# Kernel optimization log

Measured on AMD Instinct MI355X. Metric: run time of the kernel, lower is better.

## Reference

```python
import jax, jax.numpy as jnp
import numpy as np

NUM_CODES = 8192
CODE_DIM = 256
DECAY = 0.99
EPSILON = 1e-05
COMMITMENT_COST = 0.25


def setup_inputs() -> dict:
    key = jax.random.key(0)
    kz, ke = jax.random.split(key)
    z = jax.random.normal(kz, (8, 4096, CODE_DIM), dtype=jnp.float32)
    emb = jax.random.normal(ke, (NUM_CODES, CODE_DIM), dtype=jnp.float32)
    emb = emb / jnp.linalg.norm(emb, axis=1, keepdims=True)
    return {
        "z": z,
        "embedding": emb,
        "ema_cluster_size": jnp.zeros((NUM_CODES,), dtype=jnp.float32),
        "ema_embedding": emb,
    }


def reference(z, embedding, ema_cluster_size, ema_embedding):
    K, D = embedding.shape
    z_flat = z.reshape(-1, D)  # [N, D]
    # squared euclidean distances: [N, K]
    distances = (
        jnp.sum(z_flat * z_flat, axis=1, keepdims=True)
        - 2.0 * z_flat @ embedding.T
        + jnp.sum(embedding * embedding, axis=1)
    )
    indices = jnp.argmin(distances, axis=1)  # [N]
    z_q = embedding[indices]  # [N, D]

    # EMA update (training path); segment_sum replaces one-hot matmul scatter
    cluster_size = jax.ops.segment_sum(
        jnp.ones((z_flat.shape[0],), dtype=z_flat.dtype), indices, num_segments=K
    )
    new_ema_cluster_size = ema_cluster_size * DECAY + cluster_size * (1.0 - DECAY)
    dw = jax.ops.segment_sum(z_flat, indices, num_segments=K)  # [K, D]
    new_ema_embedding = ema_embedding * DECAY + dw * (1.0 - DECAY)
    n = jnp.sum(new_ema_cluster_size)
    smoothed = (new_ema_cluster_size + EPSILON) / (n + K * EPSILON) * n
    new_embedding = new_ema_embedding / smoothed[:, None]

    # straight-through (torch: z_q + (z_flat - z_q).detach())
    z_q_st = z_q + jax.lax.stop_gradient(z_flat - z_q)
    vq_loss = COMMITMENT_COST * jnp.mean((jax.lax.stop_gradient(z_q) - z_flat) ** 2)

    z_q_st = z_q_st.reshape(z.shape)
    indices = indices.reshape(z.shape[:-1])
    return (z_q_st, indices, vq_loss, new_embedding, new_ema_cluster_size, new_ema_embedding)
```

## Files before the change

### kernel.cpp

```cpp
#include <hip/hip_runtime.h>

#define NPTS   32768
#define NCODES 8192
#define DIM    256

#define DECAYF 0.99f
#define ONE_MINUS_DECAYF ((float)(1.0 - 0.99))
#define EPSF   1e-5f
#define KEPSF  ((float)(8192.0 * 1e-5))
#define MARGIN 0.05f

#define WS_PART  0
#define WS_A     (WS_PART + NPTS / 4 * 8)
#define WS_EN    (WS_A + NPTS * 4)
#define WS_CNT   (WS_EN + NCODES * 4)
#define WS_S     (WS_CNT + NCODES * 4)
#define WS_IDX   (WS_S + NCODES * 4)
#define WS_OFFS  (WS_IDX + NPTS * 4)
#define WS_CUR   (WS_OFFS + NCODES * 4)
#define WS_PLIST (WS_CUR + NCODES * 4)
#define WS_EMBT  (WS_PLIST + NPTS * 4)
#define WS_GMIN  (WS_EMBT + (size_t)DIM * NCODES * 4)
#define WS_AH    (WS_GMIN + (size_t)NPTS * 512 * 4)
#define WS_BH    (WS_AH + (size_t)NPTS * DIM * 2)

typedef __attribute__((ext_vector_type(8))) short short8;
typedef __attribute__((ext_vector_type(4))) float f32x4;

__device__ inline void gl_lds16(const void* g, void* l) {
    __builtin_amdgcn_global_load_lds(
        (const __attribute__((address_space(1))) void*)g,
        (__attribute__((address_space(3))) void*)l, 16, 0, 0);
}

__device__ inline unsigned short f2bf(float f) {
    unsigned u = __float_as_uint(f);
    return (unsigned short)((u + 0x7FFFu + ((u >> 16) & 1u)) >> 16);
}
__device__ inline unsigned f2ord(float f) {
    unsigned u = __float_as_uint(f);
    return (u & 0x80000000u) ? ~u : (u | 0x80000000u);
}

__global__ __launch_bounds__(256) void k_prep0(int* __restrict__ cnt) {
    int i = blockIdx.x * blockDim.x + threadIdx.x;
    if (i < NCODES) cnt[i] = 0;
}

__global__ __launch_bounds__(256) void k_rownorm(const float* __restrict__ x,
                                                 float* __restrict__ outn,
                                                 int nrows) {
    int w = (blockIdx.x * blockDim.x + threadIdx.x) >> 6;
    int lane = threadIdx.x & 63;
    if (w >= nrows) return;
    const float4 v = *(const float4*)(x + (size_t)w * DIM + 4 * lane);
    float q0 = v.x * v.x, q1 = v.y * v.y, q2 = v.z * v.z, q3 = v.w * v.w;
    double s = (double)q0 + (double)q1 + (double)q2 + (double)q3;
    #pragma unroll
    for (int off = 32; off > 0; off >>= 1) s += __shfl_down(s, off);
    if (lane == 0) outn[w] = (float)s;
}

__global__ __launch_bounds__(256) void k_split(const float* __restrict__ x,
                                               unsigned short* __restrict__ dst,
                                               int nelem) {
    int i = blockIdx.x * blockDim.x + threadIdx.x;
    int stride = gridDim.x * blockDim.x;
    for (int j = i; j < nelem; j += stride)
        dst[j] = f2bf(x[j]);
}

__global__ __launch_bounds__(512, 2) void k_gemm_argmin(
    const unsigned short* __restrict__ Ah,
    const unsigned short* __restrict__ Bh,
    const float* __restrict__ en,
    float* __restrict__ gmin);

template<int MH>
__device__ __forceinline__ void dsr_a(const unsigned short* LB, int wr, int l15,
                                      int l7, int quad, short8 (&af)[4][2]) {
#pragma unroll
    for (int m4 = 0; m4 < 4; ++m4) {
        const int r = wr * 128 + (MH * 4 + m4) * 16 + l15;
#pragma unroll
        for (int kk = 0; kk < 2; ++kk)
            af[m4][kk] = *(const short8*)&LB[(r * 8 + ((kk * 4 + quad) ^ l7)) * 8];
    }
}
template<int NH>
__device__ __forceinline__ void dsr_b(const unsigned short* LB, int wc, int l15,
                                      int l7, int quad, short8 (&bf)[2][2]) {
#pragma unroll
    for (int n2 = 0; n2 < 2; ++n2) {
        const int r = wc * 64 + (NH * 2 + n2) * 16 + l15;
#pragma unroll
        for (int kk = 0; kk < 2; ++kk)
            bf[n2][kk] = *(const short8*)&LB[16384 + (r * 8 + ((kk * 4 + quad) ^ l7)) * 8];
    }
}
template<int MH, int NH>
__device__ __forceinline__ void mma8(const short8 (&af)[4][2], const short8 (&bf)[2][2],
                                     f32x4 (&acc)[8][4]) {
#pragma unroll
    for (int m4 = 0; m4 < 4; ++m4)
#pragma unroll
        for (int n2 = 0; n2 < 2; ++n2)
#pragma unroll
            for (int kk = 0; kk < 2; ++kk)
                acc[MH * 4 + m4][NH * 2 + n2] = __builtin_amdgcn_mfma_f32_16x16x32_bf16(
                    af[m4][kk], bf[n2][kk], acc[MH * 4 + m4][NH * 2 + n2], 0, 0, 0);
}

__global__ __launch_bounds__(512, 2) void k_gemm_argmin(
    const unsigned short* __restrict__ Ah,
    const unsigned short* __restrict__ Bh,
    const float* __restrict__ en,
    float* __restrict__ gmin) {
    __shared__ __align__(16) unsigned short LDS[65536];

    const int t = threadIdx.x;
    const int w = t >> 6, l = t & 63;
    const int quad = l >> 4, l15 = l & 15, l7 = l & 7;
    const int wr = w >> 2, wc = w & 3;
    const int cb = blockIdx.x & 31, pb = blockIdx.x >> 5;
    const int cBase = cb * 256, pBase = pb * 256;

    const int lrs0 = t >> 3;
    const int xg = (t & 7) ^ (lrs0 & 7);
    const int rA0s0 = lrs0;
    const int rA0s1 = 128 + lrs0;
    const int rB0s0 = (lrs0 & 31) | ((lrs0 >> 5) << 6);
    const int rB0s1 = 128 + rB0s0;

    const unsigned short* gA0s0 = Bh + (size_t)(cBase + rA0s0) * DIM + xg * 8;
    const unsigned short* gA0s1 = Bh + (size_t)(cBase + rA0s1) * DIM + xg * 8;
    const unsigned short* gB0s0 = Ah + (size_t)(pBase + rB0s0) * DIM + xg * 8;
    const unsigned short* gB0s1 = Ah + (size_t)(pBase + rB0s1) * DIM + xg * 8;

    const int dA0s0 = (w * 8) * 64;
    const int dA0s1 = (128 + w * 8) * 64;
    const int dB0s0 = (((w & 3) * 8) | ((w >> 2) << 6)) * 64;
    const int dB0s1 = dB0s0 + 128 * 64;

#define STG_A0(KT, BUFS) do { \
        gl_lds16(gA0s0 + (KT) * 64, &LDS[(BUFS) + dA0s0]); \
        gl_lds16(gA0s1 + (KT) * 64, &LDS[(BUFS) + dA0s1]); } while (0)
#define STG_A1(KT, BUFS) do { \
        gl_lds16(gA0s0 + 64 * DIM + (KT) * 64, &LDS[(BUFS) + dA0s0 + 64 * 64]); \
        gl_lds16(gA0s1 + 64 * DIM + (KT) * 64, &LDS[(BUFS) + dA0s1 + 64 * 64]); } while (0)
#define STG_B0(KT, BUFS) do { \
        gl_lds16(gB0s0 + (KT) * 64, &LDS[(BUFS) + 16384 + dB0s0]); \
        gl_lds16(gB0s1 + (KT) * 64, &LDS[(BUFS) + 16384 + dB0s1]); } while (0)
#define STG_B1(KT, BUFS) do { \
        gl_lds16(gB0s0 + 32 * DIM + (KT) * 64, &LDS[(BUFS) + 16384 + dB0s0 + 32 * 64]); \
        gl_lds16(gB0s1 + 32 * DIM + (KT) * 64, &LDS[(BUFS) + 16384 + dB0s1 + 32 * 64]); } while (0)

    f32x4 acc[8][4];
#pragma unroll
    for (int i = 0; i < 8; ++i)
#pragma unroll
        for (int j = 0; j < 4; ++j) acc[i][j] = (f32x4){0.f, 0.f, 0.f, 0.f};

    STG_A0(0, 0); STG_B0(0, 0); STG_A1(0, 0); STG_B1(0, 0);
    STG_A0(1, 32768); STG_B0(1, 32768);
    asm volatile("s_waitcnt vmcnt(4)");
    __builtin_amdgcn_sched_barrier(0);
    __builtin_amdgcn_s_barrier();

    short8 af[4][2], bf0[2][2], bf1[2][2];
#pragma unroll
    for (int kt = 0; kt < 4; ++kt) {
        const unsigned short* LB = &LDS[(kt & 1) << 15];
        const int cbufS = (kt & 1) << 15;
        const int obufS = cbufS ^ 32768;
        dsr_a<0>(LB, wr, l15, l7, quad, af);
        dsr_b<0>(LB, wc, l15, l7, quad, bf0);
        if (kt + 1 < 4) STG_A1(kt + 1, obufS);
        __builtin_amdgcn_s_barrier();
        asm volatile("s_waitcnt lgkmcnt(0)");
        __builtin_amdgcn_sched_barrier(0);
        __builtin_amdgcn_s_setprio(1);
        mma8<0, 0>(af, bf0, acc);
        __builtin_amdgcn_s_setprio(0);
        __builtin_amdgcn_s_barrier();
        dsr_b<1>(LB, wc, l15, l7, quad, bf1);
        if (kt + 1 < 4) STG_B1(kt + 1, obufS);
        __builtin_amdgcn_s_barrier();
        asm volatile("s_waitcnt lgkmcnt(0)");
        __builtin_amdgcn_sched_barrier(0);
        __builtin_amdgcn_s_setprio(1);
        mma8<0, 1>(af, bf1, acc);
        __builtin_amdgcn_s_setprio(0);
        __builtin_amdgcn_s_barrier();
        dsr_a<1>(LB, wr, l15, l7, quad, af);
        if (kt + 2 < 4) STG_A0(kt + 2, cbufS);
        __builtin_amdgcn_s_barrier();
        asm volatile("s_waitcnt lgkmcnt(0)");
        __builtin_amdgcn_sched_barrier(0);
        __builtin_amdgcn_s_setprio(1);
        mma8<1, 0>(af, bf0, acc);
        __builtin_amdgcn_s_setprio(0);
        __builtin_amdgcn_s_barrier();
        if (kt + 2 < 4) STG_B0(kt + 2, cbufS);
        __builtin_amdgcn_s_barrier();
        __builtin_amdgcn_s_setprio(1);
        mma8<1, 1>(af, bf1, acc);
        __builtin_amdgcn_s_setprio(0);
        if (kt < 2) {
            asm volatile("s_waitcnt vmcnt(4)");
            __builtin_amdgcn_sched_barrier(0);
        } else if (kt == 2) {
            asm volatile("s_waitcnt vmcnt(0)");
            __builtin_amdgcn_sched_barrier(0);
        }
        __builtin_amdgcn_s_barrier();
    }
#undef STG_A0
#undef STG_A1
#undef STG_B0
#undef STG_B1

    float* outl = (float*)LDS;
#pragma unroll
    for (int m = 0; m < 8; ++m) {
        const float4 en4 = *(const float4*)&en[cBase + wr * 128 + m * 16 + quad * 4];
#pragma unroll
        for (int n = 0; n < 4; ++n) {
            f32x4 a = acc[m][n];
            float d0 = fmaf(-2.f, a[0], en4.x);
            float d1 = fmaf(-2.f, a[1], en4.y);
            float d2 = fmaf(-2.f, a[2], en4.z);
            float d3 = fmaf(-2.f, a[3], en4.w);
            float dm = fminf(fminf(d0, d1), fminf(d2, d3));
            dm = fminf(dm, __shfl_xor(dm, 16));
            dm = fminf(dm, __shfl_xor(dm, 32));
            if (quad == 0)
                outl[(wr * 8 + m) * 256 + wc * 64 + n * 16 + l15] = dm;
        }
    }
    __syncthreads();
    {
        const int pt = t >> 1, h = t & 1;
#pragma unroll
        for (int q2 = 0; q2 < 2; ++q2) {
            const int g0 = (h * 2 + q2) * 4;
            float4 v;
            v.x = outl[(g0 + 0) * 256 + pt];
            v.y = outl[(g0 + 1) * 256 + pt];
            v.z = outl[(g0 + 2) * 256 + pt];
            v.w = outl[(g0 + 3) * 256 + pt];
            *(float4*)&gmin[(size_t)(pBase + pt) * 512 + cb * 16 + g0] = v;
        }
    }
}

__global__ __launch_bounds__(256) void k_phase2(
    const float* __restrict__ z, const float* __restrict__ emb,
    const float* __restrict__ A, const float* __restrict__ en,
    const float* __restrict__ gmin,
    int* __restrict__ widx, float* __restrict__ out1,
    int* __restrict__ cnt) {
    int wpt = (blockIdx.x << 2) + (threadIdx.x >> 6);
    int l = threadIdx.x & 63;

    const float* gp = gmin + (size_t)wpt * 512;
    float loc[8];
    #pragma unroll
    for (int i = 0; i < 8; ++i) loc[i] = gp[i * 64 + l];
    float m8 = loc[0];
    #pragma unroll
    for (int i = 1; i < 8; ++i) m8 = fminf(m8, loc[i]);
    #pragma unroll
    for (int off = 1; off < 64; off <<= 1) m8 = fminf(m8, __shfl_xor(m8, off));
    const float thresh = m8 + MARGIN;

    const float4 z4 = *(const float4*)(z + (size_t)wpt * DIM + 4 * l);
    const float Azn = A[wpt];
    unsigned long long best = ~0ull;
    #pragma unroll 1
    for (int i = 0; i < 8; ++i) {
        unsigned long long mask = __ballot(loc[i] <= thresh);
        while (mask) {
            int s = __ffsll((long long)mask) - 1;
            mask &= mask - 1;
            int cbase = (i * 64 + s) << 4;
            #pragma unroll 4
            for (int k = 0; k < 16; ++k) {
                int c = cbase + k;
                const float4 ev = *(const float4*)(emb + (size_t)c * DIM + 4 * l);
                float p = fmaf(z4.x, ev.x,
                          fmaf(z4.y, ev.y,
                          fmaf(z4.z, ev.z, z4.w * ev.w)));
                #pragma unroll
                for (int off = 1; off < 64; off <<= 1) p += __shfl_xor(p, off);
                float dist = (Azn - 2.0f * p) + en[c];
                unsigned long long pk =
                    ((unsigned long long)f2ord(dist) << 32) | (unsigned)c;
                best = pk < best ? pk : best;
            }
        }
    }
    if (l == 0) {
        int idx = (int)(unsigned)best;
        widx[wpt] = idx;
        out1[wpt] = (float)idx;
        atomicAdd(cnt + idx, 1);
    }
}

__global__ __launch_bounds__(256) void k_scan(const int* __restrict__ cnt,
                                              const float* __restrict__ ecs,
                                              int* __restrict__ offs,
                                              int* __restrict__ cursor,
                                              float* __restrict__ out4,
                                              float* __restrict__ s_out) {
    __shared__ int ps[256];
    __shared__ double rd[256];
    __shared__ float nsh;
    int t = threadIdx.x;
    int base = t * 32;
    int loc[32];
    int s = 0;
    double nl = 0.0;
    #pragma unroll
    for (int i = 0; i < 32; ++i) {
        int c = cnt[base + i];
        loc[i] = c;
        s += c;
        float f = ecs[base + i] * DECAYF + (float)c * ONE_MINUS_DECAYF;
        out4[base + i] = f;
        nl += (double)f;
    }
    ps[t] = s;
    rd[t] = nl;
    __syncthreads();
    for (int off = 1; off < 256; off <<= 1) {
        int v = (t >= off) ? ps[t - off] : 0;
        __syncthreads();
        ps[t] += v;
        __syncthreads();
    }
    for (int off = 128; off > 0; off >>= 1) {
        if (t < off) rd[t] += rd[t + off];
        __syncthreads();
    }
    if (t == 0) nsh = (float)rd[0];
    __syncthreads();
    int run = (t == 0) ? 0 : ps[t - 1];
    #pragma unroll
    for (int i = 0; i < 32; ++i) {
        offs[base + i] = run;
        cursor[base + i] = run;
        run += loc[i];
    }
    float n = nsh;
    for (int k = t; k < NCODES; k += 256)
        s_out[k] = (out4[k] + EPSF) / (n + KEPSF) * n;
}

__global__ __launch_bounds__(256) void k_place(const int* __restrict__ widx,
                                               int* __restrict__ cursor,
                                               int* __restrict__ plist) {
    int p = blockIdx.x * 256 + threadIdx.x;
    int idx = widx[p];
    int slot = atomicAdd(&cursor[idx], 1);
    plist[slot] = p;
}

__global__ __launch_bounds__(256) void k_zq(const float* __restrict__ z,
                                            const float* __restrict__ emb,
                                            const int* __restrict__ widx,
                                            float* __restrict__ out0,
                                            double* __restrict__ part) {
    __shared__ double sred[4];
    int w = (blockIdx.x * blockDim.x + threadIdx.x) >> 6;
    int wv = threadIdx.x >> 6;
    int lane = threadIdx.x & 63;
    int idx = widx[w];
    const float4 zv = *(const float4*)(z + (size_t)w * DIM + 4 * lane);
    const float4 ev = *(const float4*)(emb + (size_t)idx * DIM + 4 * lane);

    float4 o;
    o.x = ev.x + (zv.x - ev.x);
    o.y = ev.y + (zv.y - ev.y);
    o.z = ev.z + (zv.z - ev.z);
    o.w = ev.w + (zv.w - ev.w);
    *(float4*)(out0 + (size_t)w * DIM + 4 * lane) = o;

    float t0 = ev.x - zv.x, t1 = ev.y - zv.y, t2 = ev.z - zv.z, t3 = ev.w - zv.w;
    float s0 = t0 * t0, s1 = t1 * t1, s2 = t2 * t2, s3 = t3 * t3;
    double ls = (double)s0 + (double)s1 + (double)s2 + (double)s3;
    #pragma unroll
    for (int off = 32; off > 0; off >>= 1) ls += __shfl_down(ls, off);
    if (lane == 0) sred[wv] = ls;
    __syncthreads();
    if (threadIdx.x == 0)
        part[blockIdx.x] = (sred[0] + sred[1]) + (sred[2] + sred[3]);
}

__global__ __launch_bounds__(256) void k_loss(const double* __restrict__ part,
                                              float* __restrict__ out2) {
    __shared__ double red[256];
    int t = threadIdx.x;
    double s = 0.0;
    for (int i = t; i < NPTS / 4; i += 256) s += part[i];
    red[t] = s;
    __syncthreads();
    for (int off = 128; off > 0; off >>= 1) {
        if (t < off) red[t] += red[t + off];
        __syncthreads();
    }
    if (t == 0)
        out2[0] = 0.25f * (float)(red[0] / (double)((size_t)NPTS * DIM));
}

__global__ __launch_bounds__(256) void k_dw(const float* __restrict__ z,
                                            const float* __restrict__ eem,
                                            const int* __restrict__ offs,
                                            const int* __restrict__ cnt,
                                            const int* __restrict__ plist,
                                            float* __restrict__ out5) {
    int c = blockIdx.x * 4 + (threadIdx.x >> 6);
    int lane = threadIdx.x & 63;
    int beg = offs[c], num = cnt[c];
    float4 acc = make_float4(0.f, 0.f, 0.f, 0.f);
    for (int j = 0; j < num; ++j) {
        int p = plist[beg + j];
        const float4 v = *(const float4*)(z + (size_t)p * DIM + 4 * lane);
        acc.x += v.x; acc.y += v.y; acc.z += v.z; acc.w += v.w;
    }
    const float4 e = *(const float4*)(eem + (size_t)c * DIM + 4 * lane);
    float4 o;
    o.x = e.x * DECAYF + acc.x * ONE_MINUS_DECAYF;
    o.y = e.y * DECAYF + acc.y * ONE_MINUS_DECAYF;
    o.z = e.z * DECAYF + acc.z * ONE_MINUS_DECAYF;
    o.w = e.w * DECAYF + acc.w * ONE_MINUS_DECAYF;
    *(float4*)(out5 + (size_t)c * DIM + 4 * lane) = o;
}

__global__ __launch_bounds__(256) void k_final(const float* __restrict__ out5,
                                               const float* __restrict__ s,
                                               float* __restrict__ out3) {
    int i = blockIdx.x * blockDim.x + threadIdx.x;
    int stride = gridDim.x * blockDim.x;
    for (int j = i; j < NCODES * DIM; j += stride)
        out3[j] = out5[j] / s[j >> 8];
}

extern "C" void kernel_launch(void* const* d_in, const int* in_sizes, int n_in,
                              void* d_out, int out_size, void* d_ws, size_t ws_size,
                              hipStream_t stream) {
    const float* z   = (const float*)d_in[0];
    const float* emb = (const float*)d_in[1];
    const float* ecs = (const float*)d_in[2];
    const float* eem = (const float*)d_in[3];

    float* out = (float*)d_out;
    float* out0 = out;
    float* out1 = out + 8388608;
    float* out2 = out + 8421376;
    float* out3 = out + 8421377;
    float* out4 = out + 10518529;
    float* out5 = out + 10526721;

    char* ws = (char*)d_ws;
    double* wPart = (double*)(ws + WS_PART);
    float*  wA    = (float*)(ws + WS_A);
    float*  wEn   = (float*)(ws + WS_EN);
    int*    wCnt  = (int*)(ws + WS_CNT);
    float*  wS    = (float*)(ws + WS_S);
    int*    wIdx  = (int*)(ws + WS_IDX);
    int*    wOffs = (int*)(ws + WS_OFFS);
    int*    wCur  = (int*)(ws + WS_CUR);
    int*    wPl   = (int*)(ws + WS_PLIST);
    float*  wGmin = (float*)(ws + WS_GMIN);
    unsigned short* wAh = (unsigned short*)(ws + WS_AH);
    unsigned short* wBh = (unsigned short*)(ws + WS_BH);

    hipLaunchKernelGGL(k_prep0, dim3(32), dim3(256), 0, stream, wCnt);
    hipLaunchKernelGGL(k_rownorm, dim3(NPTS / 4), dim3(256), 0, stream, z, wA, NPTS);
    hipLaunchKernelGGL(k_rownorm, dim3(NCODES / 4), dim3(256), 0, stream, emb, wEn, NCODES);
    hipLaunchKernelGGL(k_split, dim3(4096), dim3(256), 0, stream, z, wAh, NPTS * DIM);
    hipLaunchKernelGGL(k_split, dim3(1024), dim3(256), 0, stream, emb, wBh, NCODES * DIM);
    hipLaunchKernelGGL(k_gemm_argmin, dim3((NPTS / 256) * (NCODES / 256)), dim3(512), 0, stream,
                       wAh, wBh, wEn, wGmin);
    hipLaunchKernelGGL(k_phase2, dim3(NPTS / 4), dim3(256), 0, stream,
                       z, emb, wA, wEn, wGmin, wIdx, out1, wCnt);
    hipLaunchKernelGGL(k_scan, dim3(1), dim3(256), 0, stream,
                       wCnt, ecs, wOffs, wCur, out4, wS);
    hipLaunchKernelGGL(k_place, dim3(NPTS / 256), dim3(256), 0, stream, wIdx, wCur, wPl);
    hipLaunchKernelGGL(k_zq, dim3(NPTS / 4), dim3(256), 0, stream, z, emb, wIdx, out0, wPart);
    hipLaunchKernelGGL(k_loss, dim3(1), dim3(256), 0, stream, wPart, out2);
    hipLaunchKernelGGL(k_dw, dim3(NCODES / 4), dim3(256), 0, stream,
                       z, eem, wOffs, wCnt, wPl, out5);
    hipLaunchKernelGGL(k_final, dim3(2048), dim3(256), 0, stream, out5, wS, out3);
}
```

Baseline: 415.9 us.

## Make GEMM-argmin persistent over point tiles with cross-tile prefetch

The GEMM-argmin kernel now launches 512 blocks instead of 4096. Each block keeps one 256-code tile and walks 8 consecutive 256-point tiles, prefetching the next point tile's B data during the last k-steps of the current one. A remapped block id spreads code tiles across XCDs, and a separate LDS region holds the epilogue scratch so it does not collide with the staging buffers. The goal is to cut block launch and pipeline prologue overhead and to reuse the code tile from cache. In exchange, parallelism drops to 512 blocks at 2 per CU, which may underfill the GPU, and the epilogue now runs serially inside each block.

```diff
diff --git a/kernel.cpp b/kernel.cpp
--- a/kernel.cpp
+++ b/kernel.cpp
@@ -70,11 +70,6 @@
         dst[j] = f2bf(x[j]);
 }
 
-__global__ __launch_bounds__(512, 2) void k_gemm_argmin(
-    const unsigned short* __restrict__ Ah,
-    const unsigned short* __restrict__ Bh,
-    const float* __restrict__ en,
-    float* __restrict__ gmin);
 
 template<int MH>
 __device__ __forceinline__ void dsr_a(const unsigned short* LB, int wr, int l15,
@@ -116,14 +111,17 @@
     const unsigned short* __restrict__ Bh,
     const float* __restrict__ en,
     float* __restrict__ gmin) {
-    __shared__ __align__(16) unsigned short LDS[65536];
+    __shared__ __align__(16) unsigned short LDS[65536 + 8192];
 
     const int t = threadIdx.x;
     const int w = t >> 6, l = t & 63;
     const int quad = l >> 4, l15 = l & 15, l7 = l & 7;
     const int wr = w >> 2, wc = w & 3;
-    const int cb = blockIdx.x & 31, pb = blockIdx.x >> 5;
-    const int cBase = cb * 256, pBase = pb * 256;
+
+    const int lid = (blockIdx.x & 7) * 64 + (blockIdx.x >> 3);
+    const int cb = lid >> 4;
+    const int pbg = lid & 15;
+    const int cBase = cb * 256;
 
     const int lrs0 = t >> 3;
     const int xg = (t & 7) ^ (lrs0 & 7);
@@ -134,26 +132,26 @@
 
     const unsigned short* gA0s0 = Bh + (size_t)(cBase + rA0s0) * DIM + xg * 8;
     const unsigned short* gA0s1 = Bh + (size_t)(cBase + rA0s1) * DIM + xg * 8;
-    const unsigned short* gB0s0 = Ah + (size_t)(pBase + rB0s0) * DIM + xg * 8;
-    const unsigned short* gB0s1 = Ah + (size_t)(pBase + rB0s1) * DIM + xg * 8;
+    const unsigned short* gBs0 = Ah + (size_t)(pbg * 8 * 256 + rB0s0) * DIM + xg * 8;
+    const unsigned short* gBs1 = Ah + (size_t)(pbg * 8 * 256 + rB0s1) * DIM + xg * 8;
 
     const int dA0s0 = (w * 8) * 64;
     const int dA0s1 = (128 + w * 8) * 64;
     const int dB0s0 = (((w & 3) * 8) | ((w >> 2) << 6)) * 64;
     const int dB0s1 = dB0s0 + 128 * 64;
 
-#define STG_A0(KT, BUFS) do { \
-        gl_lds16(gA0s0 + (KT) * 64, &LDS[(BUFS) + dA0s0]); \
-        gl_lds16(gA0s1 + (KT) * 64, &LDS[(BUFS) + dA0s1]); } while (0)
-#define STG_A1(KT, BUFS) do { \
-        gl_lds16(gA0s0 + 64 * DIM + (KT) * 64, &LDS[(BUFS) + dA0s0 + 64 * 64]); \
-        gl_lds16(gA0s1 + 64 * DIM + (KT) * 64, &LDS[(BUFS) + dA0s1 + 64 * 64]); } while (0)
-#define STG_B0(KT, BUFS) do { \
-        gl_lds16(gB0s0 + (KT) * 64, &LDS[(BUFS) + 16384 + dB0s0]); \
-        gl_lds16(gB0s1 + (KT) * 64, &LDS[(BUFS) + 16384 + dB0s1]); } while (0)
-#define STG_B1(KT, BUFS) do { \
-        gl_lds16(gB0s0 + 32 * DIM + (KT) * 64, &LDS[(BUFS) + 16384 + dB0s0 + 32 * 64]); \
-        gl_lds16(gB0s1 + 32 * DIM + (KT) * 64, &LDS[(BUFS) + 16384 + dB0s1 + 32 * 64]); } while (0)
+#define STG_A0(CO, BUFS) do { \
+        gl_lds16(gA0s0 + (CO) * 64, &LDS[(BUFS) + dA0s0]); \
+        gl_lds16(gA0s1 + (CO) * 64, &LDS[(BUFS) + dA0s1]); } while (0)
+#define STG_A1(CO, BUFS) do { \
+        gl_lds16(gA0s0 + 64 * DIM + (CO) * 64, &LDS[(BUFS) + dA0s0 + 64 * 64]); \
+        gl_lds16(gA0s1 + 64 * DIM + (CO) * 64, &LDS[(BUFS) + dA0s1 + 64 * 64]); } while (0)
+#define STG_B0(P0, P1, CO, BUFS) do { \
+        gl_lds16((P0) + (CO) * 64, &LDS[(BUFS) + 16384 + dB0s0]); \
+        gl_lds16((P1) + (CO) * 64, &LDS[(BUFS) + 16384 + dB0s1]); } while (0)
+#define STG_B1(P0, P1, CO, BUFS) do { \
+        gl_lds16((P0) + 32 * DIM + (CO) * 64, &LDS[(BUFS) + 16384 + dB0s0 + 32 * 64]); \
+        gl_lds16((P1) + 32 * DIM + (CO) * 64, &LDS[(BUFS) + 16384 + dB0s1 + 32 * 64]); } while (0)
 
     f32x4 acc[8][4];
 #pragma unroll
@@ -161,97 +159,115 @@
 #pragma unroll
         for (int j = 0; j < 4; ++j) acc[i][j] = (f32x4){0.f, 0.f, 0.f, 0.f};
 
-    STG_A0(0, 0); STG_B0(0, 0); STG_A1(0, 0); STG_B1(0, 0);
-    STG_A0(1, 32768); STG_B0(1, 32768);
+    STG_A0(0, 0); STG_B0(gBs0, gBs1, 0, 0); STG_A1(0, 0); STG_B1(gBs0, gBs1, 0, 0);
+    STG_A0(1, 32768); STG_B0(gBs0, gBs1, 1, 32768);
     asm volatile("s_waitcnt vmcnt(4)");
     __builtin_amdgcn_sched_barrier(0);
     __builtin_amdgcn_s_barrier();
 
     short8 af[4][2], bf0[2][2], bf1[2][2];
-#pragma unroll
-    for (int kt = 0; kt < 4; ++kt) {
-        const unsigned short* LB = &LDS[(kt & 1) << 15];
-        const int cbufS = (kt & 1) << 15;
-        const int obufS = cbufS ^ 32768;
-        dsr_a<0>(LB, wr, l15, l7, quad, af);
-        dsr_b<0>(LB, wc, l15, l7, quad, bf0);
-        if (kt + 1 < 4) STG_A1(kt + 1, obufS);
-        __builtin_amdgcn_s_barrier();
+#pragma unroll 1
+    for (int it = 0; it < 8; ++it) {
+        const unsigned short* bt0 = gBs0 + (size_t)it * (256 * DIM);
+        const unsigned short* bt1 = gBs1 + (size_t)it * (256 * DIM);
+        const unsigned short* bn0 = bt0 + 256 * DIM;
+        const unsigned short* bn1 = bt1 + 256 * DIM;
+        const bool more = (it < 7);
+#pragma unroll
+        for (int kt = 0; kt < 4; ++kt) {
+            const int cbufS = (kt & 1) << 15;
+            const int obufS = cbufS ^ 32768;
+            const unsigned short* LB = &LDS[cbufS];
+            const int co1 = (kt + 1) & 3, co2 = (kt + 2) & 3;
+            dsr_a<0>(LB, wr, l15, l7, quad, af);
+            dsr_b<0>(LB, wc, l15, l7, quad, bf0);
+            if (kt < 3 || more) STG_A1(co1, obufS);
+            __builtin_amdgcn_s_barrier();
+            asm volatile("s_waitcnt lgkmcnt(0)");
+            __builtin_amdgcn_sched_barrier(0);
+            __builtin_amdgcn_s_setprio(1);
+            mma8<0, 0>(af, bf0, acc);
+            __builtin_amdgcn_s_setprio(0);
+            __builtin_amdgcn_s_barrier();
+            dsr_b<1>(LB, wc, l15, l7, quad, bf1);
+            if (kt < 3) { STG_B1(bt0, bt1, co1, obufS); }
+            else if (more) { STG_B1(bn0, bn1, co1, obufS); }
+            __builtin_amdgcn_s_barrier();
+            asm volatile("s_waitcnt lgkmcnt(0)");
+            __builtin_amdgcn_sched_barrier(0);
+            __builtin_amdgcn_s_setprio(1);
+            mma8<0, 1>(af, bf1, acc);
+            __builtin_amdgcn_s_setprio(0);
+            __builtin_amdgcn_s_barrier();
+            dsr_a<1>(LB, wr, l15, l7, quad, af);
+            if (kt < 2 || more) STG_A0(co2, cbufS);
+            __builtin_amdgcn_s_barrier();
+            asm volatile("s_waitcnt lgkmcnt(0)");
+            __builtin_amdgcn_sched_barrier(0);
+            __builtin_amdgcn_s_setprio(1);
+            mma8<1, 0>(af, bf0, acc);
+            __builtin_amdgcn_s_setprio(0);
+            __builtin_amdgcn_s_barrier();
+            if (kt < 2) { STG_B0(bt0, bt1, co2, cbufS); }
+            else if (more) { STG_B0(bn0, bn1, co2, cbufS); }
+            __builtin_amdgcn_s_barrier();
+            __builtin_amdgcn_s_setprio(1);
+            mma8<1, 1>(af, bf1, acc);
+            __builtin_amdgcn_s_setprio(0);
+            if (kt < 2 || more) {
+                asm volatile("s_waitcnt vmcnt(4)");
+                __builtin_amdgcn_sched_barrier(0);
+            } else if (kt == 2) {
+                asm volatile("s_waitcnt vmcnt(0)");
+                __builtin_amdgcn_sched_barrier(0);
+            }
+            __builtin_amdgcn_s_barrier();
+        }
+
+        float* outl = (float*)&LDS[65536];
+        const int pBase = (pbg * 8 + it) * 256;
+#pragma unroll
+        for (int m = 0; m < 8; ++m) {
+            const float4 en4 = *(const float4*)&en[cBase + wr * 128 + m * 16 + quad * 4];
+#pragma unroll
+            for (int n = 0; n < 4; ++n) {
+                f32x4 a = acc[m][n];
+                float d0 = fmaf(-2.f, a[0], en4.x);
+                float d1 = fmaf(-2.f, a[1], en4.y);
+                float d2 = fmaf(-2.f, a[2], en4.z);
+                float d3 = fmaf(-2.f, a[3], en4.w);
+                float dm = fminf(fminf(d0, d1), fminf(d2, d3));
+                dm = fminf(dm, __shfl_xor(dm, 16));
+                dm = fminf(dm, __shfl_xor(dm, 32));
+                if (quad == 0)
+                    outl[(wr * 8 + m) * 256 + wc * 64 + n * 16 + l15] = dm;
+            }
+        }
         asm volatile("s_waitcnt lgkmcnt(0)");
         __builtin_amdgcn_sched_barrier(0);
-        __builtin_amdgcn_s_setprio(1);
-        mma8<0, 0>(af, bf0, acc);
-        __builtin_amdgcn_s_setprio(0);
         __builtin_amdgcn_s_barrier();
-        dsr_b<1>(LB, wc, l15, l7, quad, bf1);
-        if (kt + 1 < 4) STG_B1(kt + 1, obufS);
-        __builtin_amdgcn_s_barrier();
-        asm volatile("s_waitcnt lgkmcnt(0)");
-        __builtin_amdgcn_sched_barrier(0);
-        __builtin_amdgcn_s_setprio(1);
-        mma8<0, 1>(af, bf1, acc);
-        __builtin_amdgcn_s_setprio(0);
-        __builtin_amdgcn_s_barrier();
-        dsr_a<1>(LB, wr, l15, l7, quad, af);
-        if (kt + 2 < 4) STG_A0(kt + 2, cbufS);
-        __builtin_amdgcn_s_barrier();
-        asm volatile("s_waitcnt lgkmcnt(0)");
-        __builtin_amdgcn_sched_barrier(0);
-        __builtin_amdgcn_s_setprio(1);
-        mma8<1, 0>(af, bf0, acc);
-        __builtin_amdgcn_s_setprio(0);
-        __builtin_amdgcn_s_barrier();
-        if (kt + 2 < 4) STG_B0(kt + 2, cbufS);
-        __builtin_amdgcn_s_barrier();
-        __builtin_amdgcn_s_setprio(1);
-        mma8<1, 1>(af, bf1, acc);
-        __builtin_amdgcn_s_setprio(0);
-        if (kt < 2) {
-            asm volatile("s_waitcnt vmcnt(4)");
-            __builtin_amdgcn_sched_barrier(0);
-        } else if (kt == 2) {
-            asm volatile("s_waitcnt vmcnt(0)");
-            __builtin_amdgcn_sched_barrier(0);
+        {
+            const int pt = t >> 1, h = t & 1;
+#pragma unroll
+            for (int q2 = 0; q2 < 2; ++q2) {
+                const int g0 = (h * 2 + q2) * 4;
+                float4 v;
+                v.x = outl[(g0 + 0) * 256 + pt];
+                v.y = outl[(g0 + 1) * 256 + pt];
+                v.z = outl[(g0 + 2) * 256 + pt];
+                v.w = outl[(g0 + 3) * 256 + pt];
+                *(float4*)&gmin[(size_t)(pBase + pt) * 512 + cb * 16 + g0] = v;
+            }
         }
-        __builtin_amdgcn_s_barrier();
+#pragma unroll
+        for (int i = 0; i < 8; ++i)
+#pragma unroll
+            for (int j = 0; j < 4; ++j) acc[i][j] = (f32x4){0.f, 0.f, 0.f, 0.f};
     }
 #undef STG_A0
 #undef STG_A1
 #undef STG_B0
 #undef STG_B1
-
-    float* outl = (float*)LDS;
-#pragma unroll
-    for (int m = 0; m < 8; ++m) {
-        const float4 en4 = *(const float4*)&en[cBase + wr * 128 + m * 16 + quad * 4];
-#pragma unroll
-        for (int n = 0; n < 4; ++n) {
-            f32x4 a = acc[m][n];
-            float d0 = fmaf(-2.f, a[0], en4.x);
-            float d1 = fmaf(-2.f, a[1], en4.y);
-            float d2 = fmaf(-2.f, a[2], en4.z);
-            float d3 = fmaf(-2.f, a[3], en4.w);
-            float dm = fminf(fminf(d0, d1), fminf(d2, d3));
-            dm = fminf(dm, __shfl_xor(dm, 16));
-            dm = fminf(dm, __shfl_xor(dm, 32));
-            if (quad == 0)
-                outl[(wr * 8 + m) * 256 + wc * 64 + n * 16 + l15] = dm;
-        }
-    }
-    __syncthreads();
-    {
-        const int pt = t >> 1, h = t & 1;
-#pragma unroll
-        for (int q2 = 0; q2 < 2; ++q2) {
-            const int g0 = (h * 2 + q2) * 4;
-            float4 v;
-            v.x = outl[(g0 + 0) * 256 + pt];
-            v.y = outl[(g0 + 1) * 256 + pt];
-            v.z = outl[(g0 + 2) * 256 + pt];
-            v.w = outl[(g0 + 3) * 256 + pt];
-            *(float4*)&gmin[(size_t)(pBase + pt) * 512 + cb * 16 + g0] = v;
-        }
-    }
 }
 
 __global__ __launch_bounds__(256) void k_phase2(
@@ -482,7 +498,7 @@
     hipLaunchKernelGGL(k_rownorm, dim3(NCODES / 4), dim3(256), 0, stream, emb, wEn, NCODES);
     hipLaunchKernelGGL(k_split, dim3(4096), dim3(256), 0, stream, z, wAh, NPTS * DIM);
     hipLaunchKernelGGL(k_split, dim3(1024), dim3(256), 0, stream, emb, wBh, NCODES * DIM);
-    hipLaunchKernelGGL(k_gemm_argmin, dim3((NPTS / 256) * (NCODES / 256)), dim3(512), 0, stream,
+    hipLaunchKernelGGL(k_gemm_argmin, dim3(512), dim3(512), 0, stream,
                        wAh, wBh, wEn, wGmin);
     hipLaunchKernelGGL(k_phase2, dim3(NPTS / 4), dim3(256), 0, stream,
                        z, emb, wA, wEn, wGmin, wIdx, out1, wCnt);
```

After: 511.2 us. +22.9%, slower.
